# Optimization experiments

Measured on AMD Instinct MI355X. Metric: run time of the kernel, lower is better.

The kernel has to match this reference:

```python
import jax, jax.numpy as jnp
import numpy as np

UNITS = 2048
BATCH = 4096
INPUT_DIM = 2048

def hard_sigmoid(x):
    # Keras hard_sigmoid: clip(0.2*x + 0.5, 0, 1)
    return jnp.clip(0.2 * x + 0.5, 0.0, 1.0)

def setup_inputs() -> dict:
    key = jax.random.key(0)
    ks = jax.random.split(key, 8)
    inputs = jax.random.normal(ks[0], (BATCH, INPUT_DIM), dtype=jnp.float32)
    h_tm1 = jax.random.normal(ks[1], (BATCH, UNITS), dtype=jnp.float32)
    c_tm1 = jax.random.normal(ks[2], (BATCH, UNITS), dtype=jnp.float32)
    z_tm1 = jax.random.normal(ks[3], (BATCH, UNITS), dtype=jnp.float32)
    scale = 1.0 / np.sqrt(INPUT_DIM)
    kernel = jax.random.normal(ks[4], (INPUT_DIM, 4 * UNITS), dtype=jnp.float32) * scale
    recurrent_kernel = jax.random.normal(ks[5], (UNITS, 4 * UNITS), dtype=jnp.float32) * scale
    recurrent_latent = jax.random.normal(ks[6], (UNITS, 4 * UNITS), dtype=jnp.float32) * scale
    # unit_forget_bias: bias = [zeros(units), ones(units), zeros(2*units)]
    bias = jnp.concatenate([
        jnp.zeros((UNITS,), jnp.float32),
        jnp.ones((UNITS,), jnp.float32),
        jnp.zeros((2 * UNITS,), jnp.float32),
    ])
    return {"inputs": inputs, "h_tm1": h_tm1, "c_tm1": c_tm1, "z_tm1": z_tm1,
            "kernel": kernel, "recurrent_kernel": recurrent_kernel,
            "recurrent_latent": recurrent_latent, "bias": bias}

def reference(inputs, h_tm1, c_tm1, z_tm1, kernel, recurrent_kernel, recurrent_latent, bias):
    # Fused path (implementation=2, no dropout): three matmuls + bias,
    # split into 4 gates, then gated state update.
    x = inputs @ kernel + h_tm1 @ recurrent_kernel + z_tm1 @ recurrent_latent + bias
    x_i, x_f, x_c, x_o = jnp.split(x, 4, axis=1)
    i = hard_sigmoid(x_i)
    f = hard_sigmoid(x_f)
    c = f * c_tm1 + i * jnp.tanh(x_c)
    o = hard_sigmoid(x_o)
    h = o * jnp.tanh(c)
    return h
```

## Files before the change

kernel.cpp:

```cpp
#include <hip/hip_runtime.h>
#include <hip/hip_bf16.h>

typedef float f32x4 __attribute__((ext_vector_type(4)));
typedef short short8 __attribute__((ext_vector_type(8)));
typedef short short4v __attribute__((ext_vector_type(4)));

__device__ __forceinline__ short f2b(float x) {
    union { __hip_bfloat16 b; short s; } u;
    u.b = __float2bfloat16(x);
    return u.s;
}

__device__ __forceinline__ void gload16(const void* g, void* l) {
    __builtin_amdgcn_global_load_lds(
        (const __attribute__((address_space(1))) unsigned int*)g,
        (__attribute__((address_space(3))) unsigned int*)l, 16, 0, 0);
}

__global__ __launch_bounds__(256)
void conv_a(const float* __restrict__ x0, const float* __restrict__ x1,
            const float* __restrict__ x2, unsigned short* __restrict__ Aws)
{
    const long i = (long)blockIdx.x * 256 + threadIdx.x;
    const long per_src = (long)4096 * 2048 / 8;
    const int  s = (int)(i / per_src);
    const long e0 = (i % per_src) * 8;
    const int  row = (int)(e0 >> 11), kl = (int)(e0 & 2047);
    const float* src = (s == 0) ? x0 : (s == 1) ? x1 : x2;
    const f32x4 v0 = *(const f32x4*)(src + e0);
    const f32x4 v1 = *(const f32x4*)(src + e0 + 4);
    short8 p;
    #pragma unroll
    for (int j = 0; j < 4; ++j) { p[j] = f2b(v0[j]); p[4 + j] = f2b(v1[j]); }
    *(short8*)&Aws[(long)row * 6144 + s * 2048 + kl] = p;
}

__global__ __launch_bounds__(256)
void conv_b(const float* __restrict__ Wk, const float* __restrict__ Wr,
            const float* __restrict__ Wl, unsigned short* __restrict__ Bws)
{
    __shared__ float lt[64][65];
    const int bid = (int)blockIdx.x;
    const int s   = bid >> 12;
    const int r   = bid & 4095;
    const int kbase = (r >> 7) * 64;
    const int ebase = (r & 127) * 64;
    const float* W = (s == 0) ? Wk : (s == 1) ? Wr : Wl;
    const int tr = threadIdx.x >> 4, tc = threadIdx.x & 15;

    #pragma unroll
    for (int p = 0; p < 4; ++p) {
        const int kr = p * 16 + tr;
        const f32x4 v = *(const f32x4*)&W[(long)(kbase + kr) * 8192 + ebase + tc * 4];
        #pragma unroll
        for (int j = 0; j < 4; ++j) lt[kr][tc * 4 + j] = v[j];
    }
    __syncthreads();
    #pragma unroll
    for (int p = 0; p < 4; ++p) {
        const int er = p * 16 + tr;
        const int k4 = tc * 4;
        short4v qv;
        #pragma unroll
        for (int j = 0; j < 4; ++j) qv[j] = f2b(lt[k4 + j][er]);
        *(short4v*)&Bws[(long)(ebase + er) * 6144 + (long)s * 2048 + kbase + k4] = qv;
    }
}

__global__ __launch_bounds__(512, 2)
void vlstm_gemm256(const unsigned short* __restrict__ Aws,
                   const unsigned short* __restrict__ Bws,
                   const float* __restrict__ c_tm1,
                   const float* __restrict__ bias,
                   float* __restrict__ out)
{
    __shared__ __align__(16) unsigned short As[2][256][64];
    __shared__ __align__(16) unsigned short Bs[2][256][64];

    const int tid  = threadIdx.x;
    const int w    = tid >> 6, lane = tid & 63;
    const int wm   = w >> 2,  wn   = w & 3;
    const int l15  = lane & 15, q = lane >> 4;
    const int lrow = lane >> 3;
    const int lsw  = (lane & 7) ^ lrow;
    const int oq   = q ^ (l15 & 7);

    const int bid = (int)blockIdx.x;
    const int swz = (bid & 7) * 64 + (bid >> 3);
    const int bm  = swz >> 5, bn = swz & 31;
    const int row0 = bm * 256, c0 = bn * 64;

    const long a_base = (long)(row0 + w * 16 + lrow) * 6144 + lsw * 8;

    f32x4 acc[8][4];
    #pragma unroll
    for (int mi = 0; mi < 8; ++mi)
        #pragma unroll
        for (int g = 0; g < 4; ++g)
            acc[mi][g] = (f32x4){0.f, 0.f, 0.f, 0.f};

    short8 afr[4][2];
    short8 bfr[4][2];

#define STAGE_A(buf_, t_, h_) do { _Pragma("unroll")                             \
    for (int j_ = 0; j_ < 2; ++j_)                                               \
        gload16(Aws + a_base + (long)((h_) * 128 + j_ * 8) * 6144                \
                    + (long)(t_) * 64,                                           \
                &As[buf_][(h_) * 128 + w * 16 + j_ * 8][0]); } while (0)

#define STAGE_B(buf_, t_, h_) do { _Pragma("unroll")                             \
    for (int j_ = 0; j_ < 2; ++j_) {                                             \
        const int e0_ = (h_) * 128 + w * 16 + j_ * 8;                            \
        const int grow_ = ((e0_ >> 4) & 3) * 2048 + c0 + (e0_ >> 6) * 16         \
                          + (e0_ & 8) + lrow;                                    \
        gload16(Bws + (long)grow_ * 6144 + lsw * 8 + (long)(t_) * 64,            \
                &Bs[buf_][e0_][0]); } } while (0)

#define LOAD_AFR(cur_, mh_) do { _Pragma("unroll")                               \
    for (int mi_ = 0; mi_ < 4; ++mi_) { _Pragma("unroll")                        \
        for (int kh_ = 0; kh_ < 2; ++kh_)                                        \
            afr[mi_][kh_] = *(const short8*)                                     \
                &As[cur_][wm * 128 + (mh_) * 64 + mi_ * 16 + l15]                \
                         [(oq ^ (kh_ << 2)) * 8]; } } while (0)

#define LOAD_BFR(cur_, nlo_) do { _Pragma("unroll")                              \
    for (int g_ = 0; g_ < 2; ++g_) { _Pragma("unroll")                           \
        for (int kh_ = 0; kh_ < 2; ++kh_)                                        \
            bfr[(nlo_) + g_][kh_] = *(const short8*)                             \
                &Bs[cur_][wn * 64 + ((nlo_) + g_) * 16 + l15]                    \
                         [(oq ^ (kh_ << 2)) * 8]; } } while (0)

#define MFMA_Q(mh_, nlo_) do {                                                   \
    __builtin_amdgcn_s_setprio(1);                                               \
    _Pragma("unroll")                                                            \
    for (int kh_ = 0; kh_ < 2; ++kh_) { _Pragma("unroll")                        \
        for (int mi_ = 0; mi_ < 4; ++mi_) { _Pragma("unroll")                    \
            for (int g_ = 0; g_ < 2; ++g_)                                       \
                acc[(mh_) * 4 + mi_][(nlo_) + g_] =                              \
                    __builtin_amdgcn_mfma_f32_16x16x32_bf16(                     \
                        afr[mi_][kh_], bfr[(nlo_) + g_][kh_],                    \
                        acc[(mh_) * 4 + mi_][(nlo_) + g_], 0, 0, 0); } }         \
    __builtin_amdgcn_s_setprio(0); } while (0)

#define PH_OPEN() do { __builtin_amdgcn_s_barrier();                             \
    asm volatile("s_waitcnt lgkmcnt(0)" ::: "memory");                           \
    __builtin_amdgcn_sched_barrier(0); } while (0)

#define PH_CLOSE() do { __builtin_amdgcn_s_barrier();                            \
    __builtin_amdgcn_sched_barrier(0); } while (0)

    STAGE_A(0, 0, 0); STAGE_A(0, 0, 1);
    STAGE_B(0, 0, 0); STAGE_B(0, 0, 1);
    STAGE_B(1, 1, 0); STAGE_B(1, 1, 1);
    asm volatile("s_waitcnt vmcnt(4)" ::: "memory");
    __builtin_amdgcn_s_barrier();
    __builtin_amdgcn_sched_barrier(0);

    for (int t = 0; t < 96; ++t) {
        const int cur = t & 1, nxt = cur ^ 1;
        LOAD_AFR(cur, 0);
        LOAD_BFR(cur, 0);
        if (t + 1 < 96) STAGE_A(nxt, t + 1, 0);
        PH_OPEN();
        MFMA_Q(0, 0);
        PH_CLOSE();
        LOAD_BFR(cur, 2);
        if (t + 1 < 96) STAGE_A(nxt, t + 1, 1);
        PH_OPEN();
        MFMA_Q(0, 2);
        PH_CLOSE();
        LOAD_AFR(cur, 1);
        if (t + 2 < 96) STAGE_B(cur, t + 2, 0);
        PH_OPEN();
        MFMA_Q(1, 0);
        PH_CLOSE();
        if (t + 2 < 96) STAGE_B(cur, t + 2, 1);
        PH_OPEN();
        MFMA_Q(1, 2);
        if (t < 94) asm volatile("s_waitcnt vmcnt(4)" ::: "memory");
        else        asm volatile("s_waitcnt vmcnt(0)" ::: "memory");
        PH_CLOSE();
    }

#undef STAGE_A
#undef STAGE_B
#undef LOAD_AFR
#undef LOAD_BFR
#undef MFMA_Q
#undef PH_OPEN
#undef PH_CLOSE

    {
        const int col = c0 + wn * 16 + l15;
        const float bi  = bias[col];
        const float bf_ = bias[2048 + col];
        const float bc  = bias[4096 + col];
        const float bo  = bias[6144 + col];
        #pragma unroll
        for (int mi = 0; mi < 8; ++mi) {
            const int rbase = row0 + wm * 128 + mi * 16 + q * 4;
            #pragma unroll
            for (int rr = 0; rr < 4; ++rr) {
                const int row = rbase + rr;
                const float xi = acc[mi][0][rr] + bi;
                const float xf = acc[mi][1][rr] + bf_;
                const float xc = acc[mi][2][rr] + bc;
                const float xo = acc[mi][3][rr] + bo;
                const float ig = __builtin_amdgcn_fmed3f(0.2f * xi + 0.5f, 0.f, 1.f);
                const float fg = __builtin_amdgcn_fmed3f(0.2f * xf + 0.5f, 0.f, 1.f);
                const float og = __builtin_amdgcn_fmed3f(0.2f * xo + 0.5f, 0.f, 1.f);
                const float cp = c_tm1[(long)row * 2048 + col];
                const float cc = fg * cp + ig * tanhf(xc);
                out[(long)row * 2048 + col] = og * tanhf(cc);
            }
        }
    }
}

__global__ __launch_bounds__(256, 2)
void vlstm_fused_legacy(const float* __restrict__ xin, const float* __restrict__ h_tm1,
                        const float* __restrict__ c_tm1, const float* __restrict__ z_tm1,
                        const float* __restrict__ Wk, const float* __restrict__ Wr,
                        const float* __restrict__ Wl, const float* __restrict__ bias,
                        float* __restrict__ out)
{
    __shared__ __align__(16) unsigned short Alds[2][128][40];
    __shared__ __align__(16) unsigned short Blds[2][256][40];

    const int tid  = threadIdx.x;
    const int wave = tid >> 6, lane = tid & 63;
    const int wr = wave >> 1, wc = wave & 1;
    const int l15 = lane & 15, q = lane >> 4;

    const int bid = (int)blockIdx.x;
    const int swz = (bid & 7) * 128 + (bid >> 3);
    const int bm = swz >> 5, bn = swz & 31;
    const int row0 = bm * 128, col0 = bn * 64;

    const int arow = tid >> 1, kh = tid & 1;
    const long bg_off = (long)(tid >> 6) * 2048 + col0 + (tid & 63);

    f32x4 acc[4][4][2];
    #pragma unroll
    for (int g = 0; g < 4; ++g)
        #pragma unroll
        for (int mi = 0; mi < 4; ++mi)
            #pragma unroll
            for (int ni = 0; ni < 2; ++ni)
                acc[g][mi][ni] = (f32x4){0.f, 0.f, 0.f, 0.f};

    f32x4 sa[4];
    float sb[32];

#define DO_LOADS_L(kn_) do {                                                    \
    const int s_  = (kn_) >> 6;                                                 \
    const int kl_ = ((kn_) & 63) << 5;                                          \
    const float* Ap_ = (s_ == 0) ? xin : (s_ == 1) ? h_tm1 : z_tm1;             \
    const float* Bp_ = (s_ == 0) ? Wk  : (s_ == 1) ? Wr    : Wl;                \
    const float* ap_ = Ap_ + (long)(row0 + arow) * 2048 + kl_ + kh * 16;        \
    _Pragma("unroll")                                                           \
    for (int i_ = 0; i_ < 4; ++i_) sa[i_] = ((const f32x4*)ap_)[i_];            \
    const float* bp_ = Bp_ + (long)kl_ * 8192 + bg_off;                         \
    _Pragma("unroll")                                                           \
    for (int kk_ = 0; kk_ < 32; ++kk_) sb[kk_] = bp_[(long)kk_ * 8192];         \
} while (0)

#define DO_STORE_L(buf_) do {                                                   \
    short8 p0_, p1_;                                                            \
    _Pragma("unroll")                                                           \
    for (int j_ = 0; j_ < 4; ++j_) {                                            \
        p0_[j_] = f2b(sa[0][j_]); p0_[4 + j_] = f2b(sa[1][j_]);                 \
        p1_[j_] = f2b(sa[2][j_]); p1_[4 + j_] = f2b(sa[3][j_]);                 \
    }                                                                           \
    *(short8*)&Alds[buf_][arow][kh * 16]     = p0_;                             \
    *(short8*)&Alds[buf_][arow][kh * 16 + 8] = p1_;                             \
    _Pragma("unroll")                                                           \
    for (int ks_ = 0; ks_ < 4; ++ks_) {                                         \
        short8 pb_;                                                             \
        _Pragma("unroll")                                                       \
        for (int j_ = 0; j_ < 8; ++j_) pb_[j_] = f2b(sb[ks_ * 8 + j_]);         \
        *(short8*)&Blds[buf_][tid][ks_ * 8] = pb_;                              \
    }                                                                           \
} while (0)

    DO_LOADS_L(0);
    DO_STORE_L(0);
    __syncthreads();

    for (int kt = 0; kt < 192; ++kt) {
        const int cur = kt & 1;
        if (kt + 1 < 192) DO_LOADS_L(kt + 1);

        short8 afr[4];
        #pragma unroll
        for (int mi = 0; mi < 4; ++mi)
            afr[mi] = *(const short8*)&Alds[cur][wr * 64 + mi * 16 + l15][q * 8];

        short8 bfr[4][2];
        #pragma unroll
        for (int g = 0; g < 4; ++g)
            #pragma unroll
            for (int ni = 0; ni < 2; ++ni)
                bfr[g][ni] = *(const short8*)
                    &Blds[cur][g * 64 + wc * 32 + ni * 16 + l15][q * 8];

        #pragma unroll
        for (int g = 0; g < 4; ++g)
            #pragma unroll
            for (int ni = 0; ni < 2; ++ni)
                #pragma unroll
                for (int mi = 0; mi < 4; ++mi)
                    acc[g][mi][ni] = __builtin_amdgcn_mfma_f32_16x16x32_bf16(
                        afr[mi], bfr[g][ni], acc[g][mi][ni], 0, 0, 0);

        if (kt + 1 < 192) DO_STORE_L(cur ^ 1);
        __syncthreads();
    }

#undef DO_LOADS_L
#undef DO_STORE_L

    #pragma unroll
    for (int ni = 0; ni < 2; ++ni) {
        const int col = col0 + wc * 32 + ni * 16 + l15;
        const float bi  = bias[col];
        const float bf_ = bias[2048 + col];
        const float bc  = bias[4096 + col];
        const float bo  = bias[6144 + col];
        #pragma unroll
        for (int mi = 0; mi < 4; ++mi) {
            const int rbase = row0 + wr * 64 + mi * 16 + q * 4;
            #pragma unroll
            for (int rr = 0; rr < 4; ++rr) {
                const int row = rbase + rr;
                const float xi = acc[0][mi][ni][rr] + bi;
                const float xf = acc[1][mi][ni][rr] + bf_;
                const float xc = acc[2][mi][ni][rr] + bc;
                const float xo = acc[3][mi][ni][rr] + bo;
                const float ig = __builtin_amdgcn_fmed3f(0.2f * xi + 0.5f, 0.f, 1.f);
                const float fg = __builtin_amdgcn_fmed3f(0.2f * xf + 0.5f, 0.f, 1.f);
                const float og = __builtin_amdgcn_fmed3f(0.2f * xo + 0.5f, 0.f, 1.f);
                const float cp = c_tm1[(long)row * 2048 + col];
                const float cc = fg * cp + ig * tanhf(xc);
                out[(long)row * 2048 + col] = og * tanhf(cc);
            }
        }
    }
}

extern "C" void kernel_launch(void* const* d_in, const int* in_sizes, int n_in,
                              void* d_out, int out_size, void* d_ws, size_t ws_size,
                              hipStream_t stream) {
    const float* xin  = (const float*)d_in[0];
    const float* h1   = (const float*)d_in[1];
    const float* c1   = (const float*)d_in[2];
    const float* z1   = (const float*)d_in[3];
    const float* Wk   = (const float*)d_in[4];
    const float* Wr   = (const float*)d_in[5];
    const float* Wl   = (const float*)d_in[6];
    const float* bias = (const float*)d_in[7];
    float* out = (float*)d_out;
    (void)in_sizes; (void)n_in; (void)out_size;

    const size_t a_elems = (size_t)4096 * 6144;
    const size_t b_elems = (size_t)8192 * 6144;
    const size_t need = (a_elems + b_elems) * 2;

    if (ws_size >= need) {
        unsigned short* Aws = (unsigned short*)d_ws;
        unsigned short* Bws = Aws + a_elems;
        conv_a<<<dim3(12288), dim3(256), 0, stream>>>(xin, h1, z1, Aws);
        conv_b<<<dim3(12288), dim3(256), 0, stream>>>(Wk, Wr, Wl, Bws);
        vlstm_gemm256<<<dim3(512), dim3(512), 0, stream>>>(Aws, Bws, c1, bias, out);
    } else {
        vlstm_fused_legacy<<<dim3(1024), dim3(256), 0, stream>>>(
            xin, h1, c1, z1, Wk, Wr, Wl, bias, out);
    }
}
```

Baseline: 508.3 us.

## Triple-buffer B tiles in LDS and halve barriers per K-step

The B operand's shared-memory staging grows from two buffers to three, rotating through a modulo-3 index. This lets the write for step t+2 target a buffer that no wave is still reading. The main loop drops from eight workgroup barriers and four explicit lgkmcnt(0) waits per iteration to four barriers, leaving LDS-read waits to the compiler's register-dependency tracking. The goal is less synchronisation stall between the MFMA phases. In exchange, LDS use rises to 160KB per workgroup, the full LDS capacity, and correctness now depends on the reduced barriers still ordering every reuse of the A and B buffers.

```diff
diff --git a/kernel.cpp b/kernel.cpp
--- a/kernel.cpp
+++ b/kernel.cpp
@@ -75,7 +75,7 @@
                    float* __restrict__ out)
 {
     __shared__ __align__(16) unsigned short As[2][256][64];
-    __shared__ __align__(16) unsigned short Bs[2][256][64];
+    __shared__ __align__(16) unsigned short Bs[3][256][64];
 
     const int tid  = threadIdx.x;
     const int w    = tid >> 6, lane = tid & 63;
@@ -142,44 +142,39 @@
                         acc[(mh_) * 4 + mi_][(nlo_) + g_], 0, 0, 0); } }         \
     __builtin_amdgcn_s_setprio(0); } while (0)
 
-#define PH_OPEN() do { __builtin_amdgcn_s_barrier();                             \
-    asm volatile("s_waitcnt lgkmcnt(0)" ::: "memory");                           \
-    __builtin_amdgcn_sched_barrier(0); } while (0)
-
-#define PH_CLOSE() do { __builtin_amdgcn_s_barrier();                            \
+#define BARRIER() do { __builtin_amdgcn_sched_barrier(0);                        \
+    __builtin_amdgcn_s_barrier();                                                \
     __builtin_amdgcn_sched_barrier(0); } while (0)
 
     STAGE_A(0, 0, 0); STAGE_A(0, 0, 1);
     STAGE_B(0, 0, 0); STAGE_B(0, 0, 1);
     STAGE_B(1, 1, 0); STAGE_B(1, 1, 1);
     asm volatile("s_waitcnt vmcnt(4)" ::: "memory");
-    __builtin_amdgcn_s_barrier();
-    __builtin_amdgcn_sched_barrier(0);
-
+    BARRIER();
+
+    int bB = 0;
     for (int t = 0; t < 96; ++t) {
-        const int cur = t & 1, nxt = cur ^ 1;
-        LOAD_AFR(cur, 0);
-        LOAD_BFR(cur, 0);
-        if (t + 1 < 96) STAGE_A(nxt, t + 1, 0);
-        PH_OPEN();
+        const int bA = t & 1, bAn = bA ^ 1;
+        const int bBs = bB ? bB - 1 : 2;
+        LOAD_AFR(bA, 0);
+        LOAD_BFR(bB, 0);
+        if (t + 1 < 96) STAGE_A(bAn, t + 1, 0);
+        BARRIER();
         MFMA_Q(0, 0);
-        PH_CLOSE();
-        LOAD_BFR(cur, 2);
-        if (t + 1 < 96) STAGE_A(nxt, t + 1, 1);
-        PH_OPEN();
+        LOAD_BFR(bB, 2);
+        if (t + 1 < 96) STAGE_A(bAn, t + 1, 1);
+        BARRIER();
         MFMA_Q(0, 2);
-        PH_CLOSE();
-        LOAD_AFR(cur, 1);
-        if (t + 2 < 96) STAGE_B(cur, t + 2, 0);
-        PH_OPEN();
+        LOAD_AFR(bA, 1);
+        if (t + 2 < 96) STAGE_B(bBs, t + 2, 0);
+        BARRIER();
         MFMA_Q(1, 0);
-        PH_CLOSE();
-        if (t + 2 < 96) STAGE_B(cur, t + 2, 1);
-        PH_OPEN();
+        if (t + 2 < 96) STAGE_B(bBs, t + 2, 1);
         MFMA_Q(1, 2);
         if (t < 94) asm volatile("s_waitcnt vmcnt(4)" ::: "memory");
         else        asm volatile("s_waitcnt vmcnt(0)" ::: "memory");
-        PH_CLOSE();
+        BARRIER();
+        bB = (bB == 2) ? 0 : bB + 1;
     }
 
 #undef STAGE_A
@@ -187,8 +182,7 @@
 #undef LOAD_AFR
 #undef LOAD_BFR
 #undef MFMA_Q
-#undef PH_OPEN
-#undef PH_CLOSE
+#undef BARRIER
 
     {
         const int col = c0 + wn * 16 + l15;
```

Result: no change. 509.8 us (+0.3%).
